# Kernel tuning notes

Hardware: AMD Instinct MI355X
Metric: run time of the kernel (lower is better)

Reference implementation:

```python
import jax, jax.numpy as jnp
import numpy as np

DIM = 256
HEADS = 8
HD = DIM // HEADS  # 32
RPE_H = 512
STRIDE = 16
B, NQ = 4, 300
HH, WW = 64, 64
N = HH * WW


def setup_inputs() -> dict:
    key = jax.random.key(0)
    ks = jax.random.split(key, 24)

    def lin(k, fan_in, fan_out):
        return (jax.random.normal(k, (fan_in, fan_out), jnp.float32)
                / np.float32(np.sqrt(fan_in)))

    # boxes in absolute pixel coords (image is WW*STRIDE = 1024 px wide)
    rp_xy = jax.random.uniform(ks[0], (B, NQ, 1, 2), jnp.float32) * (WW * STRIDE)
    rp_wh = jax.random.uniform(ks[1], (B, NQ, 1, 2), jnp.float32) * 256.0 + 16.0
    reference_points = jnp.concatenate([rp_xy, rp_wh], axis=-1)  # [B,NQ,1,4]

    inp = {
        "query": jax.random.normal(ks[2], (B, NQ, DIM), jnp.float32),
        "reference_points": reference_points,
        "k_input_flatten": jax.random.normal(ks[3], (B, N, DIM), jnp.float32),
        "v_input_flatten": jax.random.normal(ks[4], (B, N, DIM), jnp.float32),
        "input_spatial_shapes": jnp.array([[HH, WW]], dtype=jnp.int32),
        "input_padding_mask": (jax.random.uniform(ks[5], (B, N)) < 0.1).astype(jnp.int32),
        # projections (stored as [in, out]; y = x @ W + b)
        "Wq": lin(ks[6], DIM, DIM), "bq": jnp.zeros((DIM,), jnp.float32),
        "Wk": lin(ks[7], DIM, DIM), "bk": jnp.zeros((DIM,), jnp.float32),
        "Wv": lin(ks[8], DIM, DIM), "bv": jnp.zeros((DIM,), jnp.float32),
        "Wp": lin(ks[9], DIM, DIM), "bp": jnp.zeros((DIM,), jnp.float32),
        # CPB MLP 1 (x-deltas): Linear(2,512)+ReLU+Linear(512,HEADS,no bias)
        "W1x": lin(ks[10], 2, RPE_H), "b1x": jnp.zeros((RPE_H,), jnp.float32),
        "W2x": lin(ks[11], RPE_H, HEADS),
        # CPB MLP 2 (y-deltas)
        "W1y": lin(ks[12], 2, RPE_H), "b1y": jnp.zeros((RPE_H,), jnp.float32),
        "W2y": lin(ks[13], RPE_H, HEADS),
    }
    return inp


def reference(query, reference_points, k_input_flatten, v_input_flatten,
              input_spatial_shapes, input_padding_mask,
              Wq, bq, Wk, bk, Wv, bv, Wp, bp,
              W1x, b1x, W2x, W1y, b1y, W2y):
    h = int(input_spatial_shapes[0, 0])
    w = int(input_spatial_shapes[0, 1])
    scale = HD ** -0.5

    # cxcywh -> (x1,y1,x2,y2)
    c, s = reference_points[..., :2], reference_points[..., 2:]
    ref_pts = jnp.concatenate([c - s / 2, c + s / 2], axis=-1)  # [B,NQ,1,4]

    pos_x = (jnp.arange(w, dtype=jnp.float32) + 0.5) * STRIDE  # [w]
    pos_y = (jnp.arange(h, dtype=jnp.float32) + 0.5) * STRIDE  # [h]
    delta_x = ref_pts[..., 0::2] - pos_x[None, None, :, None]  # [B,NQ,w,2]
    delta_y = ref_pts[..., 1::2] - pos_y[None, None, :, None]  # [B,NQ,h,2]

    rpe_x = jax.nn.relu(delta_x @ W1x + b1x) @ W2x  # [B,NQ,w,HEADS]
    rpe_y = jax.nn.relu(delta_y @ W1y + b1y) @ W2y  # [B,NQ,h,HEADS]
    rpe = rpe_x[:, :, None, :, :] + rpe_y[:, :, :, None, :]  # [B,NQ,h,w,H]

    Bq, Nq, C = query.shape
    rpe = rpe.reshape(Bq, Nq, h * w, HEADS).transpose(0, 3, 1, 2)  # [B,H,NQ,N]

    q = (query @ Wq + bq).reshape(Bq, Nq, HEADS, HD).transpose(0, 2, 1, 3) * scale
    k = (k_input_flatten @ Wk + bk).reshape(Bq, -1, HEADS, HD).transpose(0, 2, 1, 3)
    v = (v_input_flatten @ Wv + bv).reshape(Bq, -1, HEADS, HD).transpose(0, 2, 1, 3)

    attn = jnp.einsum('bhqd,bhkd->bhqk', q, k) + rpe
    attn = attn + input_padding_mask[:, None, None, :].astype(attn.dtype) * (-100.0)
    fi = jnp.finfo(attn.dtype)
    attn = jnp.clip(attn, fi.min, fi.max)
    attn = jax.nn.softmax(attn, axis=-1)

    x = jnp.einsum('bhqk,bhkd->bhqd', attn, v)
    x = x.transpose(0, 2, 1, 3).reshape(Bq, Nq, C)
    return x @ Wp + bp
```

## Files before the change

kernel.cpp:

```cpp
#include <hip/hip_runtime.h>
#include <math.h>

#define B_   4
#define NQ_  300
#define DIM_ 256
#define H_   8
#define HD_  32
#define N_   4096
#define QT_  19

typedef _Float16 f16;
typedef f16   f16x8 __attribute__((ext_vector_type(8)));
typedef f16   f16x4 __attribute__((ext_vector_type(4)));
typedef float f32x4 __attribute__((ext_vector_type(4)));

#define L2E 1.44269504f

__global__ __launch_bounds__(256) void prep_wt(
    const float* __restrict__ Wq, const float* __restrict__ Wk,
    const float* __restrict__ Wv, const float* __restrict__ Wp,
    const int* __restrict__ mask, f16* __restrict__ WT,
    float* __restrict__ maskf, float qscale)
{
  const int z = blockIdx.z;
  if (z == 4) {
    const int flat = blockIdx.y * 4 + blockIdx.x;
    const int idx = flat * 1024 + threadIdx.x * 4;
    int4 mm = *(const int4*)(mask + idx);
    float4 o;
    o.x = -100.f * L2E * (float)mm.x;
    o.y = -100.f * L2E * (float)mm.y;
    o.z = -100.f * L2E * (float)mm.z;
    o.w = -100.f * L2E * (float)mm.w;
    *(float4*)(maskf + idx) = o;
    return;
  }
  __shared__ float t[64][65];
  const float* W = z == 0 ? Wq : z == 1 ? Wk : z == 2 ? Wv : Wp;
  const float s = z == 0 ? qscale : 1.0f;
  f16* O = WT + (size_t)z * 65536;
  const int k0 = blockIdx.y * 64, n0 = blockIdx.x * 64;
  const int r = threadIdx.x >> 2, c0 = (threadIdx.x & 3) * 16;
#pragma unroll
  for (int c = 0; c < 16; c += 4) {
    float4 v = *(const float4*)(W + (size_t)(k0 + r) * 256 + n0 + c0 + c);
    t[r][c0 + c] = v.x; t[r][c0 + c + 1] = v.y;
    t[r][c0 + c + 2] = v.z; t[r][c0 + c + 3] = v.w;
  }
  __syncthreads();
  f16* orow = O + (size_t)(n0 + r) * 256 + k0 + c0;
#pragma unroll
  for (int c = 0; c < 16; c += 4) {
    f16x4 p;
    p[0] = (f16)(t[c0 + c + 0][r] * s);
    p[1] = (f16)(t[c0 + c + 1][r] * s);
    p[2] = (f16)(t[c0 + c + 2][r] * s);
    p[3] = (f16)(t[c0 + c + 3][r] * s);
    *(f16x4*)(orow + c) = p;
  }
}

__device__ __forceinline__ void gemm_body(
    const void* __restrict__ Ain, const f16* __restrict__ WT,
    const float* __restrict__ bias, void* __restrict__ C,
    int M, float scale, int a_f16, int mode, int bm, int bn, int tid)
{
  __shared__ f16 As[64][40];
  __shared__ f16 Bs[64][40];
  __shared__ f16 Ts[64][72];
  const int lane = tid & 63;
  const int wv = tid >> 6;
  const int l15 = lane & 15, g = lane >> 4;
  const int arow = tid >> 2, akq = (tid & 3) * 8;

  f32x4 acc[4];
#pragma unroll
  for (int nt = 0; nt < 4; ++nt) acc[nt] = (f32x4){0.f, 0.f, 0.f, 0.f};

  for (int k0 = 0; k0 < 256; k0 += 32) {
    {
      const int gm = bm + arow;
      f16x8 av;
      if (gm < M) {
        if (a_f16) {
          av = *(const f16x8*)((const f16*)Ain + (size_t)gm * 256 + k0 + akq);
        } else {
          const float* ap = (const float*)Ain + (size_t)gm * 256 + k0 + akq;
          float4 a0 = *(const float4*)ap;
          float4 a1 = *(const float4*)(ap + 4);
          av[0] = (f16)a0.x; av[1] = (f16)a0.y; av[2] = (f16)a0.z; av[3] = (f16)a0.w;
          av[4] = (f16)a1.x; av[5] = (f16)a1.y; av[6] = (f16)a1.z; av[7] = (f16)a1.w;
        }
      } else {
#pragma unroll
        for (int i = 0; i < 8; ++i) av[i] = (f16)0.f;
      }
      *(f16x8*)&As[arow][akq] = av;
      *(f16x8*)&Bs[arow][akq] =
          *(const f16x8*)(WT + (size_t)(bn + arow) * 256 + k0 + akq);
    }
    __syncthreads();
    const f16x8 af = *(const f16x8*)&As[wv * 16 + l15][g * 8];
#pragma unroll
    for (int nt = 0; nt < 4; ++nt) {
      const f16x8 bf = *(const f16x8*)&Bs[nt * 16 + l15][g * 8];
      acc[nt] = __builtin_amdgcn_mfma_f32_16x16x32_f16(af, bf, acc[nt], 0, 0, 0);
    }
    __syncthreads();
  }

  if (mode == 2) {
#pragma unroll
    for (int nt = 0; nt < 4; ++nt) {
      const float bv = bias[bn + nt * 16 + l15];
#pragma unroll
      for (int r = 0; r < 4; ++r)
        Ts[nt * 16 + l15][wv * 16 + g * 4 + r] = (f16)(acc[nt][r] + bv);
    }
    __syncthreads();
    const int nl = tid >> 2, mc = (tid & 3) * 16;
    const int bb = bm >> 12, nk0 = bm & 4095;
    f16* dst = (f16*)C + (size_t)bb * (256 * 4096) +
               (size_t)(bn + nl) * 4096 + nk0 + mc;
    *(f16x8*)dst = *(const f16x8*)&Ts[nl][mc];
    *(f16x8*)(dst + 8) = *(const f16x8*)&Ts[nl][mc + 8];
  } else {
#pragma unroll
    for (int nt = 0; nt < 4; ++nt) {
      const int n = bn + nt * 16 + l15;
      const float bv = bias[n] * scale;
#pragma unroll
      for (int r = 0; r < 4; ++r) {
        const int m = bm + wv * 16 + g * 4 + r;
        if (m >= M) continue;
        const float v = acc[nt][r] + bv;
        if (mode == 0) ((float*)C)[(size_t)m * 256 + n] = v;
        else           ((f16*)C)[(size_t)m * 256 + n] = (f16)v;
      }
    }
  }
}

__global__ __launch_bounds__(256) void proj_qkv(
    const float* __restrict__ query, const float* __restrict__ kin,
    const float* __restrict__ vin, const f16* __restrict__ WT,
    const float* __restrict__ bq, const float* __restrict__ bk,
    const float* __restrict__ bv, f16* __restrict__ Qf,
    f16* __restrict__ Kf, f16* __restrict__ Vtf, float qscale)
{
  const int z = blockIdx.z;
  const int bm = blockIdx.y * 64, bn = blockIdx.x * 64;
  if (z == 0) {
    if (bm >= B_ * NQ_) return;
    gemm_body(query, WT, bq, Qf, B_ * NQ_, qscale, 0, 1, bm, bn, threadIdx.x);
  } else if (z == 1) {
    gemm_body(kin, WT + 65536, bk, Kf, B_ * N_, 1.0f, 0, 1, bm, bn, threadIdx.x);
  } else {
    gemm_body(vin, WT + 2 * 65536, bv, Vtf, B_ * N_, 1.0f, 0, 2, bm, bn, threadIdx.x);
  }
}

__global__ __launch_bounds__(256) void gemm_out(
    const f16* __restrict__ X, const f16* __restrict__ WT,
    const float* __restrict__ bp, float* __restrict__ out)
{
  gemm_body(X, WT + 3 * 65536, bp, out, B_ * NQ_, 1.0f, 1, 0,
            blockIdx.y * 64, blockIdx.x * 64, threadIdx.x);
}

__global__ __launch_bounds__(256) void rpe_kernel(
    const float* __restrict__ refpts,
    const float* __restrict__ W1x, const float* __restrict__ b1x, const float* __restrict__ W2x,
    const float* __restrict__ W1y, const float* __restrict__ b1y, const float* __restrict__ W2y,
    float* __restrict__ rpxT, float* __restrict__ rpyT)
{
  __shared__ float sRed[4][64][9];
  const int tid = threadIdx.x;
  const int lane = tid & 63;
  const int wv = __builtin_amdgcn_readfirstlane(tid >> 6);
  const int bq = blockIdx.x;
  const int axis = blockIdx.y;
  const float* W1 = axis ? W1y : W1x;
  const float* b1 = axis ? b1y : b1x;
  const float* W2 = axis ? W2y : W2x;
  float* out = axis ? rpyT : rpxT;
  const int b = bq / NQ_, q = bq % NQ_;

  const float c  = refpts[bq * 4 + axis];
  const float sz = refpts[bq * 4 + 2 + axis];
  const float pos = (lane + 0.5f) * 16.0f;
  const float d0 = c - 0.5f * sz - pos;
  const float d1 = c + 0.5f * sz - pos;
  float acc[8] = {};
  const int r0 = wv * 128;
#pragma unroll 4
  for (int i = 0; i < 128; ++i) {
    const int r = r0 + i;
    const float w10 = W1[r], w11 = W1[512 + r], bb = b1[r];
    const float hv = fmaxf(fmaf(d0, w10, fmaf(d1, w11, bb)), 0.0f);
    const float* w2r = W2 + r * 8;
#pragma unroll
    for (int hh = 0; hh < 8; ++hh) acc[hh] += hv * w2r[hh];
  }
#pragma unroll
  for (int hh = 0; hh < 8; ++hh) sRed[wv][lane][hh] = acc[hh];
  __syncthreads();
  for (int idx = tid; idx < 512; idx += 256) {
    const int hh = idx >> 6, jj = idx & 63;
    out[((size_t)(b * H_ + hh) * NQ_ + q) * 64 + jj] =
        (sRed[0][jj][hh] + sRed[1][jj][hh] + sRed[2][jj][hh] + sRed[3][jj][hh]) * L2E;
  }
}

__global__ __launch_bounds__(512, 4) void attn_mfma(
    const f16* __restrict__ Qf, const f16* __restrict__ Kf,
    const f16* __restrict__ Vtf, const float* __restrict__ rpxT,
    const float* __restrict__ rpyT, const float* __restrict__ maskf,
    f16* __restrict__ X)
{
  __shared__ float srx[16][68];
  __shared__ float sry[16][68];
  __shared__ f16x4 mO4[7][2][64];
  __shared__ float mlm[7][16];
  __shared__ float mll[7][16];

  const int tid = threadIdx.x;
  const int lane = tid & 63;
  const int kh = tid >> 6;
  const int qb = blockIdx.x % QT_;
  const int h  = (blockIdx.x / QT_) % H_;
  const int b  = blockIdx.x / (QT_ * H_);
  const int q0 = qb * 16;

  {
    const int t = tid & 255;
    const int qq = t >> 4, j4 = t & 15;
    int qg = q0 + qq; if (qg > NQ_ - 1) qg = NQ_ - 1;
    const float* src = (tid < 256 ? rpxT : rpyT) +
        ((size_t)((b * H_ + h) * NQ_ + qg)) * 64 + j4 * 4;
    float4 v = *(const float4*)src;
    float* dst = (tid < 256) ? &srx[qq][j4 * 4] : &sry[qq][j4 * 4];
    *(float4*)dst = v;
  }
  __syncthreads();

  const int l15 = lane & 15, g = lane >> 4;
  const int qrow = q0 + l15;
  const int qc = qrow > NQ_ - 1 ? NQ_ - 1 : qrow;
  const f16x8 qf = *(const f16x8*)(Qf + (size_t)(b * NQ_ + qc) * 256 + h * 32 + g * 8);

  f32x4 O0 = {0.f, 0.f, 0.f, 0.f}, O1 = {0.f, 0.f, 0.f, 0.f};
  float lacc = 0.f, mrun = -1e30f;
  const f16* kb  = Kf + (size_t)b * N_ * 256 + h * 32 + g * 8;
  const f16* v0p = Vtf + (size_t)(b * 256 + h * 32 + l15) * N_ + g * 4;
  const f16* v1p = v0p + (size_t)16 * N_;
  const float* mb = maskf + b * N_;

  for (int sp = 0; sp < 8; ++sp) {
    const int kbase = kh * 512 + sp * 64;
    f16x8 kf[4]; f16x4 va[4], vb[4]; float4 m4[4];
#pragma unroll
    for (int cc = 0; cc < 4; ++cc) {
      kf[cc] = *(const f16x8*)(kb + (size_t)(kbase + cc * 16 + l15) * 256);
      va[cc] = *(const f16x4*)(v0p + kbase + cc * 16);
      vb[cc] = *(const f16x4*)(v1p + kbase + cc * 16);
      m4[cc] = *(const float4*)(mb + kbase + cc * 16 + g * 4);
    }
    const float ryc = sry[l15][kbase >> 6];
    f32x4 s[4];
    float lm = -1e30f;
#pragma unroll
    for (int cc = 0; cc < 4; ++cc) {
      f32x4 S = __builtin_amdgcn_mfma_f32_16x16x32_f16(
          kf[cc], qf, (f32x4){0.f, 0.f, 0.f, 0.f}, 0, 0, 0);
      const float4 rx = *(const float4*)&srx[l15][cc * 16 + g * 4];
      s[cc][0] = fmaf(S[0], L2E, rx.x + m4[cc].x + ryc);
      s[cc][1] = fmaf(S[1], L2E, rx.y + m4[cc].y + ryc);
      s[cc][2] = fmaf(S[2], L2E, rx.z + m4[cc].z + ryc);
      s[cc][3] = fmaf(S[3], L2E, rx.w + m4[cc].w + ryc);
      lm = fmaxf(lm, fmaxf(fmaxf(s[cc][0], s[cc][1]), fmaxf(s[cc][2], s[cc][3])));
    }
    lm = fmaxf(lm, __shfl_xor(lm, 16));
    lm = fmaxf(lm, __shfl_xor(lm, 32));
    const float mn = fmaxf(mrun, lm);
    const float fr = exp2f(mrun - mn);
    mrun = mn;
    lacc *= fr;
#pragma unroll
    for (int r = 0; r < 4; ++r) { O0[r] *= fr; O1[r] *= fr; }
#pragma unroll
    for (int cc = 0; cc < 4; ++cc) {
      f16x4 pf;
#pragma unroll
      for (int r = 0; r < 4; ++r) {
        const float p = exp2f(s[cc][r] - mrun);
        lacc += p;
        pf[r] = (f16)p;
      }
      O0 = __builtin_amdgcn_mfma_f32_16x16x16f16(va[cc], pf, O0, 0, 0, 0);
      O1 = __builtin_amdgcn_mfma_f32_16x16x16f16(vb[cc], pf, O1, 0, 0, 0);
    }
  }
  lacc += __shfl_xor(lacc, 16);
  lacc += __shfl_xor(lacc, 32);

  if (kh > 0) {
    f16x4 pa, pb;
#pragma unroll
    for (int r = 0; r < 4; ++r) { pa[r] = (f16)O0[r]; pb[r] = (f16)O1[r]; }
    mO4[kh - 1][0][lane] = pa;
    mO4[kh - 1][1][lane] = pb;
    if (lane < 16) { mlm[kh - 1][lane] = mrun; mll[kh - 1][lane] = lacc; }
  }
  __syncthreads();
  if (kh == 0) {
    float ms = mrun;
#pragma unroll
    for (int w = 0; w < 7; ++w) ms = fmaxf(ms, mlm[w][l15]);
    const float f0 = exp2f(mrun - ms);
    float lt = lacc * f0;
    float fw[7];
#pragma unroll
    for (int w = 0; w < 7; ++w) {
      fw[w] = exp2f(mlm[w][l15] - ms);
      lt += mll[w][l15] * fw[w];
    }
    const float rl = 1.0f / lt;
    if (qrow < NQ_) {
      f16* xr = X + (size_t)(b * NQ_ + qrow) * 256 + h * 32;
      f16x4 p0, p1;
#pragma unroll
      for (int r = 0; r < 4; ++r) {
        float o0 = O0[r] * f0, o1 = O1[r] * f0;
#pragma unroll
        for (int w = 0; w < 7; ++w) {
          o0 += (float)mO4[w][0][lane][r] * fw[w];
          o1 += (float)mO4[w][1][lane][r] * fw[w];
        }
        p0[r] = (f16)(o0 * rl);
        p1[r] = (f16)(o1 * rl);
      }
      *(f16x4*)(xr + g * 4) = p0;
      *(f16x4*)(xr + 16 + g * 4) = p1;
    }
  }
}

extern "C" void kernel_launch(void* const* d_in, const int* in_sizes, int n_in,
                              void* d_out, int out_size, void* d_ws, size_t ws_size,
                              hipStream_t stream)
{
  const float* query  = (const float*)d_in[0];
  const float* refpts = (const float*)d_in[1];
  const float* kin    = (const float*)d_in[2];
  const float* vin    = (const float*)d_in[3];
  const int*   mask   = (const int*)d_in[5];
  const float* Wq = (const float*)d_in[6];
  const float* bq = (const float*)d_in[7];
  const float* Wk = (const float*)d_in[8];
  const float* bk = (const float*)d_in[9];
  const float* Wv = (const float*)d_in[10];
  const float* bv = (const float*)d_in[11];
  const float* Wp = (const float*)d_in[12];
  const float* bp = (const float*)d_in[13];
  const float* W1x = (const float*)d_in[14];
  const float* b1x = (const float*)d_in[15];
  const float* W2x = (const float*)d_in[16];
  const float* W1y = (const float*)d_in[17];
  const float* b1y = (const float*)d_in[18];
  const float* W2y = (const float*)d_in[19];

  char* wsb = (char*)d_ws;
  f16*   Qf    = (f16*)(wsb);
  f16*   Kf    = (f16*)(wsb + 622592);
  f16*   Vtf   = (f16*)(wsb + 9011200);
  float* rpxT  = (float*)(wsb + 17399808);
  float* rpyT  = (float*)(wsb + 19857408);
  f16*   X     = (f16*)(wsb + 22315008);
  f16*   WT    = (f16*)(wsb + 22937600);
  float* maskf = (float*)(wsb + 23461888);

  const float scale = 0.17677669529663687f;

  hipLaunchKernelGGL(prep_wt, dim3(4, 4, 5), dim3(256), 0, stream,
                     Wq, Wk, Wv, Wp, mask, WT, maskf, scale);
  hipLaunchKernelGGL(rpe_kernel, dim3(B_ * NQ_, 2), dim3(256), 0, stream,
                     refpts, W1x, b1x, W2x, W1y, b1y, W2y, rpxT, rpyT);
  hipLaunchKernelGGL(proj_qkv, dim3(4, 256, 3), dim3(256), 0, stream,
                     query, kin, vin, WT, bq, bk, bv, Qf, Kf, Vtf, scale);
  hipLaunchKernelGGL(attn_mfma, dim3(B_ * H_ * QT_), dim3(512), 0, stream,
                     Qf, Kf, Vtf, rpxT, rpyT, maskf, X);
  hipLaunchKernelGGL(gemm_out, dim3(4, 19), dim3(256), 0, stream,
                     X, WT, bp, (float*)d_out);
}
```

Before: 241.5 us.

## Double M-tile in GEMMs and use two-pass softmax with 32 queries per attention block

The projection GEMMs now compute 128x64 tiles per block, with each wave owning two 16-row MFMA tiles, so every B-tile load is reused twice. The attention kernel handles 32 queries per block so each K/V fetch serves two query tiles. It also replaces the online softmax with a two-pass scheme: a first pass over all keys computes the exact row max, and a second pass does exp and accumulation without rescaling, which makes the cross-wave merge a plain sum. The cost is recomputing QK^T twice, fewer blocks in the grid (320 attention blocks), and higher register pressure.

```diff
diff --git a/kernel.cpp b/kernel.cpp
--- a/kernel.cpp
+++ b/kernel.cpp
@@ -7,7 +7,6 @@
 #define H_   8
 #define HD_  32
 #define N_   4096
-#define QT_  19
 
 typedef _Float16 f16;
 typedef f16   f16x8 __attribute__((ext_vector_type(8)));
@@ -63,29 +62,33 @@
 __device__ __forceinline__ void gemm_body(
     const void* __restrict__ Ain, const f16* __restrict__ WT,
     const float* __restrict__ bias, void* __restrict__ C,
-    int M, float scale, int a_f16, int mode, int bm, int bn, int tid)
-{
-  __shared__ f16 As[64][40];
+    int M, int a_f16, int mode, int bm, int bn, int tid)
+{
+  __shared__ f16 As[128][40];
   __shared__ f16 Bs[64][40];
-  __shared__ f16 Ts[64][72];
+  __shared__ f16 Ts[64][132];
   const int lane = tid & 63;
   const int wv = tid >> 6;
   const int l15 = lane & 15, g = lane >> 4;
-  const int arow = tid >> 2, akq = (tid & 3) * 8;
-
-  f32x4 acc[4];
-#pragma unroll
-  for (int nt = 0; nt < 4; ++nt) acc[nt] = (f32x4){0.f, 0.f, 0.f, 0.f};
+
+  f32x4 acc[2][4];
+#pragma unroll
+  for (int mt = 0; mt < 2; ++mt)
+#pragma unroll
+    for (int nt = 0; nt < 4; ++nt) acc[mt][nt] = (f32x4){0.f, 0.f, 0.f, 0.f};
 
   for (int k0 = 0; k0 < 256; k0 += 32) {
-    {
-      const int gm = bm + arow;
+#pragma unroll
+    for (int i = 0; i < 2; ++i) {
+      const int c = tid + i * 256;
+      const int row = c >> 2, k8 = (c & 3) * 8;
+      const int gm = bm + row;
       f16x8 av;
       if (gm < M) {
         if (a_f16) {
-          av = *(const f16x8*)((const f16*)Ain + (size_t)gm * 256 + k0 + akq);
+          av = *(const f16x8*)((const f16*)Ain + (size_t)gm * 256 + k0 + k8);
         } else {
-          const float* ap = (const float*)Ain + (size_t)gm * 256 + k0 + akq;
+          const float* ap = (const float*)Ain + (size_t)gm * 256 + k0 + k8;
           float4 a0 = *(const float4*)ap;
           float4 a1 = *(const float4*)(ap + 4);
           av[0] = (f16)a0.x; av[1] = (f16)a0.y; av[2] = (f16)a0.z; av[3] = (f16)a0.w;
@@ -93,18 +96,22 @@
         }
       } else {
 #pragma unroll
-        for (int i = 0; i < 8; ++i) av[i] = (f16)0.f;
-      }
-      *(f16x8*)&As[arow][akq] = av;
-      *(f16x8*)&Bs[arow][akq] =
-          *(const f16x8*)(WT + (size_t)(bn + arow) * 256 + k0 + akq);
+        for (int j = 0; j < 8; ++j) av[j] = (f16)0.f;
+      }
+      *(f16x8*)&As[row][k8] = av;
+    }
+    {
+      const int n = tid >> 2, k8 = (tid & 3) * 8;
+      *(f16x8*)&Bs[n][k8] = *(const f16x8*)(WT + (size_t)(bn + n) * 256 + k0 + k8);
     }
     __syncthreads();
-    const f16x8 af = *(const f16x8*)&As[wv * 16 + l15][g * 8];
+    const f16x8 af0 = *(const f16x8*)&As[wv * 32 + l15][g * 8];
+    const f16x8 af1 = *(const f16x8*)&As[wv * 32 + 16 + l15][g * 8];
 #pragma unroll
     for (int nt = 0; nt < 4; ++nt) {
       const f16x8 bf = *(const f16x8*)&Bs[nt * 16 + l15][g * 8];
-      acc[nt] = __builtin_amdgcn_mfma_f32_16x16x32_f16(af, bf, acc[nt], 0, 0, 0);
+      acc[0][nt] = __builtin_amdgcn_mfma_f32_16x16x32_f16(af0, bf, acc[0][nt], 0, 0, 0);
+      acc[1][nt] = __builtin_amdgcn_mfma_f32_16x16x32_f16(af1, bf, acc[1][nt], 0, 0, 0);
     }
     __syncthreads();
   }
@@ -114,26 +121,31 @@
     for (int nt = 0; nt < 4; ++nt) {
       const float bv = bias[bn + nt * 16 + l15];
 #pragma unroll
-      for (int r = 0; r < 4; ++r)
-        Ts[nt * 16 + l15][wv * 16 + g * 4 + r] = (f16)(acc[nt][r] + bv);
+      for (int mt = 0; mt < 2; ++mt)
+#pragma unroll
+        for (int r = 0; r < 4; ++r)
+          Ts[nt * 16 + l15][wv * 32 + mt * 16 + g * 4 + r] = (f16)(acc[mt][nt][r] + bv);
     }
     __syncthreads();
-    const int nl = tid >> 2, mc = (tid & 3) * 16;
+    const int n = tid >> 2, mc = (tid & 3) * 32;
     const int bb = bm >> 12, nk0 = bm & 4095;
     f16* dst = (f16*)C + (size_t)bb * (256 * 4096) +
-               (size_t)(bn + nl) * 4096 + nk0 + mc;
-    *(f16x8*)dst = *(const f16x8*)&Ts[nl][mc];
-    *(f16x8*)(dst + 8) = *(const f16x8*)&Ts[nl][mc + 8];
+               (size_t)(bn + n) * 4096 + nk0 + mc;
+#pragma unroll
+    for (int j = 0; j < 4; ++j)
+      *(f16x8*)(dst + j * 8) = *(const f16x8*)&Ts[n][mc + j * 8];
   } else {
 #pragma unroll
     for (int nt = 0; nt < 4; ++nt) {
       const int n = bn + nt * 16 + l15;
-      const float bv = bias[n] * scale;
+      const float bv = bias[n];
+#pragma unroll
+      for (int mt = 0; mt < 2; ++mt)
 #pragma unroll
       for (int r = 0; r < 4; ++r) {
-        const int m = bm + wv * 16 + g * 4 + r;
+        const int m = bm + wv * 32 + mt * 16 + g * 4 + r;
         if (m >= M) continue;
-        const float v = acc[nt][r] + bv;
+        const float v = acc[mt][nt][r] + bv;
         if (mode == 0) ((float*)C)[(size_t)m * 256 + n] = v;
         else           ((f16*)C)[(size_t)m * 256 + n] = (f16)v;
       }
@@ -146,17 +158,17 @@
     const float* __restrict__ vin, const f16* __restrict__ WT,
     const float* __restrict__ bq, const float* __restrict__ bk,
     const float* __restrict__ bv, f16* __restrict__ Qf,
-    f16* __restrict__ Kf, f16* __restrict__ Vtf, float qscale)
+    f16* __restrict__ Kf, f16* __restrict__ Vtf)
 {
   const int z = blockIdx.z;
-  const int bm = blockIdx.y * 64, bn = blockIdx.x * 64;
+  const int bm = blockIdx.y * 128, bn = blockIdx.x * 64;
   if (z == 0) {
     if (bm >= B_ * NQ_) return;
-    gemm_body(query, WT, bq, Qf, B_ * NQ_, qscale, 0, 1, bm, bn, threadIdx.x);
+    gemm_body(query, WT, bq, Qf, B_ * NQ_, 0, 1, bm, bn, threadIdx.x);
   } else if (z == 1) {
-    gemm_body(kin, WT + 65536, bk, Kf, B_ * N_, 1.0f, 0, 1, bm, bn, threadIdx.x);
+    gemm_body(kin, WT + 65536, bk, Kf, B_ * N_, 0, 1, bm, bn, threadIdx.x);
   } else {
-    gemm_body(vin, WT + 2 * 65536, bv, Vtf, B_ * N_, 1.0f, 0, 2, bm, bn, threadIdx.x);
+    gemm_body(vin, WT + 2 * 65536, bv, Vtf, B_ * N_, 0, 2, bm, bn, threadIdx.x);
   }
 }
 
@@ -164,8 +176,8 @@
     const f16* __restrict__ X, const f16* __restrict__ WT,
     const float* __restrict__ bp, float* __restrict__ out)
 {
-  gemm_body(X, WT + 3 * 65536, bp, out, B_ * NQ_, 1.0f, 1, 0,
-            blockIdx.y * 64, blockIdx.x * 64, threadIdx.x);
+  gemm_body(X, WT + 3 * 65536, bp, out, B_ * NQ_, 1, 0,
+            blockIdx.y * 128, blockIdx.x * 64, threadIdx.x);
 }
 
 __global__ __launch_bounds__(256) void rpe_kernel(
@@ -218,44 +230,89 @@
     const float* __restrict__ rpyT, const float* __restrict__ maskf,
     f16* __restrict__ X)
 {
-  __shared__ float srx[16][68];
-  __shared__ float sry[16][68];
-  __shared__ f16x4 mO4[7][2][64];
-  __shared__ float mlm[7][16];
-  __shared__ float mll[7][16];
+  __shared__ float srx[32][68];
+  __shared__ float sry[32][68];
+  __shared__ float pm[8][2][64];
+  __shared__ f16x4 mO4[7][4][64];
+  __shared__ float mll[7][32];
 
   const int tid = threadIdx.x;
   const int lane = tid & 63;
   const int kh = tid >> 6;
-  const int qb = blockIdx.x % QT_;
-  const int h  = (blockIdx.x / QT_) % H_;
-  const int b  = blockIdx.x / (QT_ * H_);
-  const int q0 = qb * 16;
+  const int qg = blockIdx.x % 10;
+  const int h  = (blockIdx.x / 10) % H_;
+  const int b  = blockIdx.x / (10 * H_);
+  const int q0 = qg * 32;
 
   {
-    const int t = tid & 255;
-    const int qq = t >> 4, j4 = t & 15;
-    int qg = q0 + qq; if (qg > NQ_ - 1) qg = NQ_ - 1;
-    const float* src = (tid < 256 ? rpxT : rpyT) +
-        ((size_t)((b * H_ + h) * NQ_ + qg)) * 64 + j4 * 4;
-    float4 v = *(const float4*)src;
-    float* dst = (tid < 256) ? &srx[qq][j4 * 4] : &sry[qq][j4 * 4];
-    *(float4*)dst = v;
+    const int qq = tid >> 4, j4 = tid & 15;
+    int qa = q0 + qq; if (qa > NQ_ - 1) qa = NQ_ - 1;
+    const size_t base = ((size_t)((b * H_ + h) * NQ_ + qa)) * 64 + j4 * 4;
+    *(float4*)&srx[qq][j4 * 4] = *(const float4*)(rpxT + base);
+    *(float4*)&sry[qq][j4 * 4] = *(const float4*)(rpyT + base);
   }
   __syncthreads();
 
   const int l15 = lane & 15, g = lane >> 4;
-  const int qrow = q0 + l15;
-  const int qc = qrow > NQ_ - 1 ? NQ_ - 1 : qrow;
-  const f16x8 qf = *(const f16x8*)(Qf + (size_t)(b * NQ_ + qc) * 256 + h * 32 + g * 8);
-
-  f32x4 O0 = {0.f, 0.f, 0.f, 0.f}, O1 = {0.f, 0.f, 0.f, 0.f};
-  float lacc = 0.f, mrun = -1e30f;
+  const int qrow0 = q0 + l15;
+  const int qrow1 = q0 + 16 + l15;
+  const int qa = qrow0 > NQ_ - 1 ? NQ_ - 1 : qrow0;
+  const int qb = qrow1 > NQ_ - 1 ? NQ_ - 1 : qrow1;
+
+  const f16x8 qf0 = *(const f16x8*)(Qf + (size_t)(b * NQ_ + qa) * 256 + h * 32 + g * 8);
+  const f16x8 qf1 = *(const f16x8*)(Qf + (size_t)(b * NQ_ + qb) * 256 + h * 32 + g * 8);
+
   const f16* kb  = Kf + (size_t)b * N_ * 256 + h * 32 + g * 8;
   const f16* v0p = Vtf + (size_t)(b * 256 + h * 32 + l15) * N_ + g * 4;
   const f16* v1p = v0p + (size_t)16 * N_;
   const float* mb = maskf + b * N_;
 
+  float cmax0 = -1e30f, cmax1 = -1e30f;
+  for (int sp = 0; sp < 8; ++sp) {
+    const int kbase = kh * 512 + sp * 64;
+    f16x8 kf[4]; float4 m4[4];
+#pragma unroll
+    for (int cc = 0; cc < 4; ++cc) {
+      kf[cc] = *(const f16x8*)(kb + (size_t)(kbase + cc * 16 + l15) * 256);
+      m4[cc] = *(const float4*)(mb + kbase + cc * 16 + g * 4);
+    }
+    const float ry0 = sry[l15][kbase >> 6];
+    const float ry1 = sry[16 + l15][kbase >> 6];
+#pragma unroll
+    for (int cc = 0; cc < 4; ++cc) {
+      f32x4 S0 = __builtin_amdgcn_mfma_f32_16x16x32_f16(
+          kf[cc], qf0, (f32x4){0.f, 0.f, 0.f, 0.f}, 0, 0, 0);
+      f32x4 S1 = __builtin_amdgcn_mfma_f32_16x16x32_f16(
+          kf[cc], qf1, (f32x4){0.f, 0.f, 0.f, 0.f}, 0, 0, 0);
+      const float4 rx0 = *(const float4*)&srx[l15][cc * 16 + g * 4];
+      const float4 rx1 = *(const float4*)&srx[16 + l15][cc * 16 + g * 4];
+      cmax0 = fmaxf(cmax0, fmaxf(
+          fmaxf(fmaf(S0[0], L2E, rx0.x + m4[cc].x + ry0),
+                fmaf(S0[1], L2E, rx0.y + m4[cc].y + ry0)),
+          fmaxf(fmaf(S0[2], L2E, rx0.z + m4[cc].z + ry0),
+                fmaf(S0[3], L2E, rx0.w + m4[cc].w + ry0))));
+      cmax1 = fmaxf(cmax1, fmaxf(
+          fmaxf(fmaf(S1[0], L2E, rx1.x + m4[cc].x + ry1),
+                fmaf(S1[1], L2E, rx1.y + m4[cc].y + ry1)),
+          fmaxf(fmaf(S1[2], L2E, rx1.z + m4[cc].z + ry1),
+                fmaf(S1[3], L2E, rx1.w + m4[cc].w + ry1))));
+    }
+  }
+  pm[kh][0][lane] = cmax0;
+  pm[kh][1][lane] = cmax1;
+  __syncthreads();
+  float m0 = -1e30f, m1 = -1e30f;
+#pragma unroll
+  for (int w = 0; w < 8; ++w)
+#pragma unroll
+    for (int gg = 0; gg < 4; ++gg) {
+      m0 = fmaxf(m0, pm[w][0][gg * 16 + l15]);
+      m1 = fmaxf(m1, pm[w][1][gg * 16 + l15]);
+    }
+
+  f32x4 O00 = {0.f,0.f,0.f,0.f}, O01 = {0.f,0.f,0.f,0.f};
+  f32x4 O10 = {0.f,0.f,0.f,0.f}, O11 = {0.f,0.f,0.f,0.f};
+  float lacc0 = 0.f, lacc1 = 0.f;
   for (int sp = 0; sp < 8; ++sp) {
     const int kbase = kh * 512 + sp * 64;
     f16x8 kf[4]; f16x4 va[4], vb[4]; float4 m4[4];
@@ -266,79 +323,96 @@
       vb[cc] = *(const f16x4*)(v1p + kbase + cc * 16);
       m4[cc] = *(const float4*)(mb + kbase + cc * 16 + g * 4);
     }
-    const float ryc = sry[l15][kbase >> 6];
-    f32x4 s[4];
-    float lm = -1e30f;
+    const float ry0 = sry[l15][kbase >> 6] - m0;
+    const float ry1 = sry[16 + l15][kbase >> 6] - m1;
 #pragma unroll
     for (int cc = 0; cc < 4; ++cc) {
-      f32x4 S = __builtin_amdgcn_mfma_f32_16x16x32_f16(
-          kf[cc], qf, (f32x4){0.f, 0.f, 0.f, 0.f}, 0, 0, 0);
-      const float4 rx = *(const float4*)&srx[l15][cc * 16 + g * 4];
-      s[cc][0] = fmaf(S[0], L2E, rx.x + m4[cc].x + ryc);
-      s[cc][1] = fmaf(S[1], L2E, rx.y + m4[cc].y + ryc);
-      s[cc][2] = fmaf(S[2], L2E, rx.z + m4[cc].z + ryc);
-      s[cc][3] = fmaf(S[3], L2E, rx.w + m4[cc].w + ryc);
-      lm = fmaxf(lm, fmaxf(fmaxf(s[cc][0], s[cc][1]), fmaxf(s[cc][2], s[cc][3])));
-    }
-    lm = fmaxf(lm, __shfl_xor(lm, 16));
-    lm = fmaxf(lm, __shfl_xor(lm, 32));
-    const float mn = fmaxf(mrun, lm);
-    const float fr = exp2f(mrun - mn);
-    mrun = mn;
-    lacc *= fr;
-#pragma unroll
-    for (int r = 0; r < 4; ++r) { O0[r] *= fr; O1[r] *= fr; }
-#pragma unroll
-    for (int cc = 0; cc < 4; ++cc) {
-      f16x4 pf;
-#pragma unroll
-      for (int r = 0; r < 4; ++r) {
-        const float p = exp2f(s[cc][r] - mrun);
-        lacc += p;
-        pf[r] = (f16)p;
-      }
-      O0 = __builtin_amdgcn_mfma_f32_16x16x16f16(va[cc], pf, O0, 0, 0, 0);
-      O1 = __builtin_amdgcn_mfma_f32_16x16x16f16(vb[cc], pf, O1, 0, 0, 0);
-    }
-  }
-  lacc += __shfl_xor(lacc, 16);
-  lacc += __shfl_xor(lacc, 32);
+      f32x4 S0 = __builtin_amdgcn_mfma_f32_16x16x32_f16(
+          kf[cc], qf0, (f32x4){0.f, 0.f, 0.f, 0.f}, 0, 0, 0);
+      f32x4 S1 = __builtin_amdgcn_mfma_f32_16x16x32_f16(
+          kf[cc], qf1, (f32x4){0.f, 0.f, 0.f, 0.f}, 0, 0, 0);
+      const float4 rx0 = *(const float4*)&srx[l15][cc * 16 + g * 4];
+      const float4 rx1 = *(const float4*)&srx[16 + l15][cc * 16 + g * 4];
+      f16x4 pf0, pf1;
+      {
+        const float p0 = exp2f(fmaf(S0[0], L2E, rx0.x + m4[cc].x + ry0));
+        const float p1 = exp2f(fmaf(S0[1], L2E, rx0.y + m4[cc].y + ry0));
+        const float p2 = exp2f(fmaf(S0[2], L2E, rx0.z + m4[cc].z + ry0));
+        const float p3 = exp2f(fmaf(S0[3], L2E, rx0.w + m4[cc].w + ry0));
+        lacc0 += p0 + p1 + p2 + p3;
+        pf0[0] = (f16)p0; pf0[1] = (f16)p1; pf0[2] = (f16)p2; pf0[3] = (f16)p3;
+      }
+      {
+        const float p0 = exp2f(fmaf(S1[0], L2E, rx1.x + m4[cc].x + ry1));
+        const float p1 = exp2f(fmaf(S1[1], L2E, rx1.y + m4[cc].y + ry1));
+        const float p2 = exp2f(fmaf(S1[2], L2E, rx1.z + m4[cc].z + ry1));
+        const float p3 = exp2f(fmaf(S1[3], L2E, rx1.w + m4[cc].w + ry1));
+        lacc1 += p0 + p1 + p2 + p3;
+        pf1[0] = (f16)p0; pf1[1] = (f16)p1; pf1[2] = (f16)p2; pf1[3] = (f16)p3;
+      }
+      O00 = __builtin_amdgcn_mfma_f32_16x16x16f16(va[cc], pf0, O00, 0, 0, 0);
+      O01 = __builtin_amdgcn_mfma_f32_16x16x16f16(vb[cc], pf0, O01, 0, 0, 0);
+      O10 = __builtin_amdgcn_mfma_f32_16x16x16f16(va[cc], pf1, O10, 0, 0, 0);
+      O11 = __builtin_amdgcn_mfma_f32_16x16x16f16(vb[cc], pf1, O11, 0, 0, 0);
+    }
+  }
+  lacc0 += __shfl_xor(lacc0, 16); lacc0 += __shfl_xor(lacc0, 32);
+  lacc1 += __shfl_xor(lacc1, 16); lacc1 += __shfl_xor(lacc1, 32);
 
   if (kh > 0) {
-    f16x4 pa, pb;
-#pragma unroll
-    for (int r = 0; r < 4; ++r) { pa[r] = (f16)O0[r]; pb[r] = (f16)O1[r]; }
-    mO4[kh - 1][0][lane] = pa;
-    mO4[kh - 1][1][lane] = pb;
-    if (lane < 16) { mlm[kh - 1][lane] = mrun; mll[kh - 1][lane] = lacc; }
+    f16x4 t;
+#pragma unroll
+    for (int r = 0; r < 4; ++r) t[r] = (f16)O00[r];
+    mO4[kh - 1][0][lane] = t;
+#pragma unroll
+    for (int r = 0; r < 4; ++r) t[r] = (f16)O01[r];
+    mO4[kh - 1][1][lane] = t;
+#pragma unroll
+    for (int r = 0; r < 4; ++r) t[r] = (f16)O10[r];
+    mO4[kh - 1][2][lane] = t;
+#pragma unroll
+    for (int r = 0; r < 4; ++r) t[r] = (f16)O11[r];
+    mO4[kh - 1][3][lane] = t;
+    if (lane < 16) {
+      mll[kh - 1][lane]      = lacc0;
+      mll[kh - 1][16 + lane] = lacc1;
+    }
   }
   __syncthreads();
   if (kh == 0) {
-    float ms = mrun;
-#pragma unroll
-    for (int w = 0; w < 7; ++w) ms = fmaxf(ms, mlm[w][l15]);
-    const float f0 = exp2f(mrun - ms);
-    float lt = lacc * f0;
-    float fw[7];
+    float lt0 = lacc0, lt1 = lacc1;
 #pragma unroll
     for (int w = 0; w < 7; ++w) {
-      fw[w] = exp2f(mlm[w][l15] - ms);
-      lt += mll[w][l15] * fw[w];
-    }
-    const float rl = 1.0f / lt;
-    if (qrow < NQ_) {
-      f16* xr = X + (size_t)(b * NQ_ + qrow) * 256 + h * 32;
+      lt0 += mll[w][l15];
+      lt1 += mll[w][16 + l15];
+#pragma unroll
+      for (int r = 0; r < 4; ++r) {
+        O00[r] += (float)mO4[w][0][lane][r];
+        O01[r] += (float)mO4[w][1][lane][r];
+        O10[r] += (float)mO4[w][2][lane][r];
+        O11[r] += (float)mO4[w][3][lane][r];
+      }
+    }
+    const float rl0 = 1.0f / lt0;
+    const float rl1 = 1.0f / lt1;
+    if (qrow0 < NQ_) {
+      f16* xr = X + (size_t)(b * NQ_ + qrow0) * 256 + h * 32;
       f16x4 p0, p1;
 #pragma unroll
       for (int r = 0; r < 4; ++r) {
-        float o0 = O0[r] * f0, o1 = O1[r] * f0;
-#pragma unroll
-        for (int w = 0; w < 7; ++w) {
-          o0 += (float)mO4[w][0][lane][r] * fw[w];
-          o1 += (float)mO4[w][1][lane][r] * fw[w];
-        }
-        p0[r] = (f16)(o0 * rl);
-        p1[r] = (f16)(o1 * rl);
+        p0[r] = (f16)(O00[r] * rl0);
+        p1[r] = (f16)(O01[r] * rl0);
+      }
+      *(f16x4*)(xr + g * 4) = p0;
+      *(f16x4*)(xr + 16 + g * 4) = p1;
+    }
+    if (qrow1 < NQ_) {
+      f16* xr = X + (size_t)(b * NQ_ + qrow1) * 256 + h * 32;
+      f16x4 p0, p1;
+#pragma unroll
+      for (int r = 0; r < 4; ++r) {
+        p0[r] = (f16)(O10[r] * rl1);
+        p1[r] = (f16)(O11[r] * rl1);
       }
       *(f16x4*)(xr + g * 4) = p0;
       *(f16x4*)(xr + 16 + g * 4) = p1;
@@ -372,13 +446,13 @@
 
   char* wsb = (char*)d_ws;
   f16*   Qf    = (f16*)(wsb);
-  f16*   Kf    = (f16*)(wsb + 622592);
-  f16*   Vtf   = (f16*)(wsb + 9011200);
-  float* rpxT  = (float*)(wsb + 17399808);
-  float* rpyT  = (float*)(wsb + 19857408);
-  f16*   X     = (f16*)(wsb + 22315008);
-  f16*   WT    = (f16*)(wsb + 22937600);
-  float* maskf = (float*)(wsb + 23461888);
+  f16*   Kf    = (f16*)(wsb + 655360);
+  f16*   Vtf   = (f16*)(wsb + 9043968);
+  float* rpxT  = (float*)(wsb + 17432576);
+  float* rpyT  = (float*)(wsb + 19890176);
+  f16*   X     = (f16*)(wsb + 22347776);
+  f16*   WT    = (f16*)(wsb + 23003136);
+  float* maskf = (float*)(wsb + 23527424);
 
   const float scale = 0.17677669529663687f;
 
@@ -386,10 +460,10 @@
                      Wq, Wk, Wv, Wp, mask, WT, maskf, scale);
   hipLaunchKernelGGL(rpe_kernel, dim3(B_ * NQ_, 2), dim3(256), 0, stream,
                      refpts, W1x, b1x, W2x, W1y, b1y, W2y, rpxT, rpyT);
-  hipLaunchKernelGGL(proj_qkv, dim3(4, 256, 3), dim3(256), 0, stream,
-                     query, kin, vin, WT, bq, bk, bv, Qf, Kf, Vtf, scale);
-  hipLaunchKernelGGL(attn_mfma, dim3(B_ * H_ * QT_), dim3(512), 0, stream,
+  hipLaunchKernelGGL(proj_qkv, dim3(4, 128, 3), dim3(256), 0, stream,
+                     query, kin, vin, WT, bq, bk, bv, Qf, Kf, Vtf);
+  hipLaunchKernelGGL(attn_mfma, dim3(B_ * H_ * 10), dim3(512), 0, stream,
                      Qf, Kf, Vtf, rpxT, rpyT, maskf, X);
-  hipLaunchKernelGGL(gemm_out, dim3(4, 19), dim3(256), 0, stream,
+  hipLaunchKernelGGL(gemm_out, dim3(4, 10), dim3(256), 0, stream,
                      X, WT, bp, (float*)d_out);
 }
```

Result: slower. 251.2 us (+4.0%).
